# Performance work log

Measured on AMD Instinct MI355X. Metric: run time of the kernel, lower is better.

Reference implementation:

```python
import jax, jax.numpy as jnp
import numpy as np

B, N, DIN, DOUT = 8, 2048, 512, 256
NUM_BUCKETS = 20


def setup_inputs() -> dict:
    key = jax.random.key(0)
    ks = jax.random.split(key, 12)
    s_in = 1.0 / np.sqrt(DIN)
    s_out = 1.0 / np.sqrt(DOUT)
    return {
        "x": jax.random.normal(ks[0], (B, N, DIN), dtype=jnp.float32),
        "price_rank": jax.random.randint(ks[1], (B, N), 0, N, dtype=jnp.int64),
        "Wq": jax.random.uniform(ks[2], (DOUT, DIN), jnp.float32, -s_in, s_in),
        "bq": jax.random.uniform(ks[3], (DOUT,), jnp.float32, -s_in, s_in),
        "Wk": jax.random.uniform(ks[4], (DOUT, DIN), jnp.float32, -s_in, s_in),
        "bk": jax.random.uniform(ks[5], (DOUT,), jnp.float32, -s_in, s_in),
        "Wv": jax.random.uniform(ks[6], (DOUT, DIN), jnp.float32, -s_in, s_in),
        "bv": jax.random.uniform(ks[7], (DOUT,), jnp.float32, -s_in, s_in),
        "Ws": jax.random.uniform(ks[8], (1, DOUT), jnp.float32, -s_out, s_out),
        "bs": jax.random.uniform(ks[9], (1,), jnp.float32, -s_out, s_out),
        "rank_emb": jax.random.normal(ks[10], (NUM_BUCKETS, 1), dtype=jnp.float32),
        "rank_w": jnp.ones((1,), dtype=jnp.float32),
    }


def reference(x, price_rank, Wq, bq, Wk, bk, Wv, bv, Ws, bs, rank_emb, rank_w):
    scale = jnp.sqrt(jnp.asarray(DOUT, dtype=x.dtype))
    q = jnp.einsum("bnd,od->bno", x, Wq) + bq  # [B,N,DOUT]
    k = jnp.einsum("bnd,od->bno", x, Wk) + bk
    v = jnp.einsum("bnd,od->bno", x, Wv) + bv
    scores = jnp.einsum("bno,bmo->bnm", q, k) / scale  # [B,N,N]
    # learned pairwise rank-distance bias gate
    rank_dist = jnp.abs(price_rank[:, :, None] - price_rank[:, None, :])
    buckets = jnp.clip(rank_dist // 5, 0, NUM_BUCKETS - 1)  # [B,N,N] int
    prior = rank_emb[buckets, 0]  # gather embedding, squeeze last dim
    gate = jax.nn.sigmoid(rank_w[0] * prior)
    scores = scores * gate
    attn = jax.nn.softmax(scores, axis=2)
    context = jnp.einsum("bnm,bmo->bno", attn, v)  # [B,N,DOUT]
    winner = jax.nn.sigmoid(jnp.einsum("bno,uo->bnu", context, Ws) + bs)[..., 0]
    return winner  # [B,N]
```

## Files before the change

### kernel.cpp

```cpp
#include <hip/hip_runtime.h>
#include <hip/hip_bf16.h>

#define B_    8
#define N_    2048
#define DIN_  512
#define DOUT_ 256
#define NBUCK 20

typedef __attribute__((ext_vector_type(8))) short  short8;
typedef __attribute__((ext_vector_type(4))) float  floatx4;

__device__ __forceinline__ unsigned short f2b(float f) {
    __hip_bfloat16 h = __float2bfloat16(f);
    unsigned short u;
    __builtin_memcpy(&u, &h, 2);
    return u;
}

__device__ __forceinline__ void load_lds16(const unsigned short* g, unsigned short* l) {
    __builtin_amdgcn_global_load_lds(
        (const __attribute__((address_space(1))) unsigned int*)g,
        (__attribute__((address_space(3))) unsigned int*)l, 16, 0, 0);
}

__device__ __forceinline__ float fexp2(float x) {
    float r;
    asm("v_exp_f32 %0, %1" : "=v"(r) : "v"(x));
    return r;
}

__global__ __launch_bounds__(256) void prep_kernel(
    const float* __restrict__ Wv, const float* __restrict__ Ws,
    const float* __restrict__ bv,
    float* __restrict__ wvs, float* __restrict__ bvs) {
    const int blk = blockIdx.x, tid = threadIdx.x;
    __shared__ float wsl[DOUT_];
    wsl[tid] = Ws[tid];
    __syncthreads();
    if (tid < 128) {
        int d = blk * 128 + tid;
        float s0 = 0.f, s1 = 0.f, s2 = 0.f, s3 = 0.f;
#pragma unroll 8
        for (int o = 0; o < DOUT_; o += 4) {
            s0 += Wv[(size_t)(o + 0) * DIN_ + d] * wsl[o + 0];
            s1 += Wv[(size_t)(o + 1) * DIN_ + d] * wsl[o + 1];
            s2 += Wv[(size_t)(o + 2) * DIN_ + d] * wsl[o + 2];
            s3 += Wv[(size_t)(o + 3) * DIN_ + d] * wsl[o + 3];
        }
        wvs[d] = (s0 + s1) + (s2 + s3);
    }
    if (blk == 0 && tid < 64) {
        float bb = wsl[tid] * bv[tid] + wsl[tid + 64] * bv[tid + 64] +
                   wsl[tid + 128] * bv[tid + 128] + wsl[tid + 192] * bv[tid + 192];
        for (int off = 1; off < 64; off <<= 1) bb += __shfl_xor(bb, off, 64);
        if (tid == 0) *bvs = bb;
    }
}

__global__ __launch_bounds__(256) void cvt_x_kernel(const float* __restrict__ x,
                                                    const float* __restrict__ wvs,
                                                    const float* __restrict__ bvs,
                                                    const float* __restrict__ wq,
                                                    const float* __restrict__ wk,
                                                    unsigned short* __restrict__ xb,
                                                    unsigned short* __restrict__ wdst,
                                                    float* __restrict__ vw) {
    int tid = threadIdx.x;
    if (blockIdx.x >= 4096) {
        int i = ((blockIdx.x - 4096) * 256 + tid) * 8;
        const float* src = (i < 131072) ? (wq + i) : (wk + (i - 131072));
        float4 a = *(const float4*)(src);
        float4 b = *(const float4*)(src + 4);
        uint4 r;
        r.x = f2b(a.x) | ((unsigned)f2b(a.y) << 16);
        r.y = f2b(a.z) | ((unsigned)f2b(a.w) << 16);
        r.z = f2b(b.x) | ((unsigned)f2b(b.y) << 16);
        r.w = f2b(b.z) | ((unsigned)f2b(b.w) << 16);
        *(uint4*)(wdst + i) = r;
        return;
    }
    int wave = tid >> 6, lane = tid & 63;
    int row = blockIdx.x * 4 + wave;
    size_t base = (size_t)row * DIN_ + lane * 8;
    float4 a = *(const float4*)(x + base);
    float4 b = *(const float4*)(x + base + 4);
    float4 wa = *(const float4*)(wvs + lane * 8);
    float4 wb = *(const float4*)(wvs + lane * 8 + 4);
    uint4 r;
    r.x = f2b(a.x) | ((unsigned)f2b(a.y) << 16);
    r.y = f2b(a.z) | ((unsigned)f2b(a.w) << 16);
    r.z = f2b(b.x) | ((unsigned)f2b(b.y) << 16);
    r.w = f2b(b.z) | ((unsigned)f2b(b.w) << 16);
    *(uint4*)(xb + base) = r;
    float d = a.x * wa.x + a.y * wa.y + a.z * wa.z + a.w * wa.w +
              b.x * wb.x + b.y * wb.y + b.z * wb.z + b.w * wb.w;
    for (int off = 1; off < 64; off <<= 1) d += __shfl_xor(d, off, 64);
    if (lane == 0) vw[row] = d + *bvs;
}

__global__ __launch_bounds__(256, 2) void qkv_kernel(
    const unsigned short* __restrict__ xb, const unsigned short* __restrict__ wb,
    const float* __restrict__ bq, const float* __restrict__ bk,
    unsigned short* __restrict__ qo, unsigned short* __restrict__ ko) {
    __shared__ unsigned short alds[2][128 * 64];
    __shared__ unsigned short blds[2][128 * 64];
    const int g = blockIdx.x;
    const int xcd = g & 7, t2 = g >> 3;
    const int colBlk = t2 & 3, rowGrp = t2 >> 2;
    const int rowBlk = rowGrp * 8 + xcd;
    const int tid = threadIdx.x;
    const int wave = tid >> 6, lane = tid & 63, quad = lane >> 4, l16 = lane & 15;
    const int wr = wave >> 1, wc = wave & 1;
    const int row0 = rowBlk * 128, col0 = colBlk * 128;
    const int sw3 = l16 & 7;

    floatx4 acc[4][4];
#pragma unroll
    for (int i = 0; i < 4; ++i)
#pragma unroll
        for (int j = 0; j < 4; ++j) acc[i][j] = (floatx4){0.f, 0.f, 0.f, 0.f};

    const int gseg = (lane & 7) ^ (lane >> 3);
    const unsigned short* ag = xb + (size_t)(row0 + wave * 8 + (lane >> 3)) * DIN_ + gseg * 8;
    const unsigned short* bg = wb + (size_t)(col0 + wave * 8 + (lane >> 3)) * DIN_ + gseg * 8;

#pragma unroll
    for (int i = 0; i < 4; ++i) {
        load_lds16(ag + (size_t)i * 32 * DIN_, &alds[0][wave * 512 + i * 2048]);
        load_lds16(bg + (size_t)i * 32 * DIN_, &blds[0][wave * 512 + i * 2048]);
    }
    __syncthreads();

#pragma unroll 1
    for (int t = 0; t < 8; ++t) {
        const unsigned short* al = (t & 1) ? alds[1] : alds[0];
        const unsigned short* bl = (t & 1) ? blds[1] : blds[0];
        unsigned short* aln = (t & 1) ? &alds[0][0] : &alds[1][0];
        unsigned short* bln = (t & 1) ? &blds[0][0] : &blds[1][0];
        if (t < 7) {
            size_t koff = (size_t)(t + 1) * 64;
#pragma unroll
            for (int i = 0; i < 4; ++i) {
                load_lds16(ag + (size_t)i * 32 * DIN_ + koff, aln + wave * 512 + i * 2048);
                load_lds16(bg + (size_t)i * 32 * DIN_ + koff, bln + wave * 512 + i * 2048);
            }
        }
#pragma unroll
        for (int h = 0; h < 2; ++h) {
            short8 af[4], bf[4];
#pragma unroll
            for (int f = 0; f < 4; ++f) {
                int ar = wr * 64 + f * 16 + l16;
                int br = wc * 64 + f * 16 + l16;
                int s  = (h * 4 + quad) ^ sw3;
                af[f] = *(const short8*)&al[(size_t)ar * 64 + s * 8];
                bf[f] = *(const short8*)&bl[(size_t)br * 64 + s * 8];
            }
#pragma unroll
            for (int i = 0; i < 4; ++i)
#pragma unroll
                for (int j = 0; j < 4; ++j)
                    acc[i][j] = __builtin_amdgcn_mfma_f32_16x16x32_bf16(af[i], bf[j], acc[i][j], 0, 0, 0);
        }
        __syncthreads();
    }

#pragma unroll
    for (int j = 0; j < 4; ++j) {
        int col = col0 + wc * 64 + j * 16 + l16;
        unsigned short* dst = (col < 256) ? qo : ko;
        float bias = (col < 256) ? bq[col] : bk[col - 256];
        int c = col & 255;
#pragma unroll
        for (int i = 0; i < 4; ++i)
#pragma unroll
            for (int r = 0; r < 4; ++r) {
                int row = row0 + wr * 64 + i * 16 + quad * 4 + r;
                dst[(size_t)row * DOUT_ + c] = f2b(acc[i][j][r] + bias);
            }
    }
}

__global__ __launch_bounds__(512, 2) void attn_kernel(
    const unsigned short* __restrict__ q, const unsigned short* __restrict__ k,
    const float* __restrict__ vw, const int* __restrict__ pr,
    const float* __restrict__ rank_emb, const float* __restrict__ rank_w,
    const float* __restrict__ bs, float* __restrict__ out) {
    const int g = blockIdx.x;
    const int b = g & 7, rblk = g >> 3;
    const int tid = threadIdx.x, wave = tid >> 6, lane = tid & 63;
    const int quad = lane >> 4, l16 = lane & 15;
    const int n0 = rblk * 64;
    const int sw = l16 & 7;

    __shared__ unsigned short klds[2][8][4096];
    __shared__ float gtab[NBUCK];
    __shared__ float lL[8][64], wdL[8][64];

    if (tid < NBUCK)
        gtab[tid] = 0.0625f * 1.44269504f / (1.f + __expf(-rank_w[0] * rank_emb[tid]));
    __syncthreads();

    const unsigned short* qb = q + (size_t)b * N_ * DOUT_;
    const unsigned short* kb = k + (size_t)b * N_ * DOUT_;
    const float* vwb = vw + b * N_;
    const int* prb = pr + b * N_;

    short8 qf[4][8];
#pragma unroll
    for (int a = 0; a < 4; ++a)
#pragma unroll
        for (int c = 0; c < 8; ++c)
            qf[a][c] = *(const short8*)(qb + (size_t)(n0 + a * 16 + l16) * DOUT_ + c * 32 + quad * 8);

    float prn5[4][4];
#pragma unroll
    for (int a = 0; a < 4; ++a)
#pragma unroll
        for (int r = 0; r < 4; ++r)
            prn5[a][r] = (float)prb[n0 + a * 16 + quad * 4 + r] * 0.2f;

    float lacc[4][4], wacc[4][4];
#pragma unroll
    for (int a = 0; a < 4; ++a)
#pragma unroll
        for (int r = 0; r < 4; ++r) { lacc[a][r] = 0.f; wacc[a][r] = 0.f; }

    const int srow = lane >> 5;
    const int spos = lane & 31;
    const unsigned short* kwb = kb + (size_t)(wave * 16) * DOUT_;
    unsigned short* buf0 = &klds[0][wave][0];
    unsigned short* buf1 = &klds[1][wave][0];
    const int colbase = wave * 16 + l16;

    int   prm_raw = prb[colbase];
    float vwv_cur = vwb[colbase];

#pragma unroll
    for (int i = 0; i < 8; ++i) {
        int row = i * 2 + srow;
        int gseg = spos ^ (row & 7);
        load_lds16(kwb + (size_t)row * DOUT_ + gseg * 8, buf0 + i * 512);
    }

#pragma unroll 1
    for (int j = 0; j < 16; ++j) {
        unsigned short* bufc = (j & 1) ? buf1 : buf0;
        unsigned short* bufn = (j & 1) ? buf0 : buf1;

        floatx4 s[4];
#pragma unroll
        for (int a = 0; a < 4; ++a) s[a] = (floatx4){0.f, 0.f, 0.f, 0.f};
        __builtin_amdgcn_s_setprio(1);
#pragma unroll
        for (int c = 0; c < 8; ++c) {
            int seg = (quad + 4 * c) ^ sw;
            short8 kf = *(const short8*)&bufc[((size_t)l16 * 32 + seg) * 8];
            s[0] = __builtin_amdgcn_mfma_f32_16x16x32_bf16(qf[0][c], kf, s[0], 0, 0, 0);
            s[1] = __builtin_amdgcn_mfma_f32_16x16x32_bf16(qf[1][c], kf, s[1], 0, 0, 0);
            s[2] = __builtin_amdgcn_mfma_f32_16x16x32_bf16(qf[2][c], kf, s[2], 0, 0, 0);
            s[3] = __builtin_amdgcn_mfma_f32_16x16x32_bf16(qf[3][c], kf, s[3], 0, 0, 0);
        }
        __builtin_amdgcn_s_setprio(0);
        int nxtcol = ((j < 15) ? (j + 1) * 128 : j * 128) + colbase;
        int   prm_nxt = prb[nxtcol];
        float vwv_nxt = vwb[nxtcol];
        if (j < 15) {
            const unsigned short* src = kwb + (size_t)(j + 1) * 128 * DOUT_;
#pragma unroll
            for (int i = 0; i < 8; ++i) {
                int row = i * 2 + srow;
                int gseg = spos ^ (row & 7);
                load_lds16(src + (size_t)row * DOUT_ + gseg * 8, bufn + i * 512);
            }
        }
        float prm5 = (float)prm_raw * 0.2f;
#pragma unroll
        for (int a = 0; a < 4; ++a)
#pragma unroll
            for (int r = 0; r < 4; ++r) {
                float d5 = fabsf(prn5[a][r] - prm5);
                int idx = (int)fminf(d5, 19.0f);
                float p = fexp2(s[a][r] * gtab[idx]);
                lacc[a][r] += p;
                wacc[a][r] += p * vwv_cur;
            }
        prm_raw = prm_nxt;
        vwv_cur = vwv_nxt;
    }

#pragma unroll
    for (int off = 1; off < 16; off <<= 1) {
#pragma unroll
        for (int a = 0; a < 4; ++a)
#pragma unroll
            for (int r = 0; r < 4; ++r) {
                lacc[a][r] += __shfl_xor(lacc[a][r], off, 64);
                wacc[a][r] += __shfl_xor(wacc[a][r], off, 64);
            }
    }
    if (l16 == 0) {
#pragma unroll
        for (int a = 0; a < 4; ++a)
#pragma unroll
            for (int r = 0; r < 4; ++r) {
                int row = a * 16 + quad * 4 + r;
                lL[wave][row]  = lacc[a][r];
                wdL[wave][row] = wacc[a][r];
            }
    }
    __syncthreads();
    if (tid < 64) {
        float l = 0.f, wd = 0.f;
#pragma unroll
        for (int s2 = 0; s2 < 8; ++s2) { l += lL[s2][tid]; wd += wdL[s2][tid]; }
        float logit = wd / l + bs[0];
        out[(size_t)b * N_ + n0 + tid] = 1.f / (1.f + __expf(-logit));
    }
}

extern "C" void kernel_launch(void* const* d_in, const int* in_sizes, int n_in,
                              void* d_out, int out_size, void* d_ws, size_t ws_size,
                              hipStream_t stream) {
    const float* x   = (const float*)d_in[0];
    const int*   pr  = (const int*)d_in[1];
    const float* Wq  = (const float*)d_in[2];
    const float* bq  = (const float*)d_in[3];
    const float* Wk  = (const float*)d_in[4];
    const float* bk  = (const float*)d_in[5];
    const float* Wv  = (const float*)d_in[6];
    const float* bv  = (const float*)d_in[7];
    const float* Ws  = (const float*)d_in[8];
    const float* bs  = (const float*)d_in[9];
    const float* remb = (const float*)d_in[10];
    const float* rw   = (const float*)d_in[11];
    float* out = (float*)d_out;

    char* ws = (char*)d_ws;
    unsigned short* xb  = (unsigned short*)ws;
    unsigned short* wb  = (unsigned short*)(ws + 16777216);
    unsigned short* q   = (unsigned short*)(ws + 17301504);
    unsigned short* kk  = (unsigned short*)(ws + 25690112);
    float*          vwp = (float*)(ws + 34078720);
    float*          wvs = (float*)(ws + 34144256);
    float*          bvs = (float*)(ws + 34146304);

    hipLaunchKernelGGL(prep_kernel, dim3(4), dim3(256), 0, stream,
                       Wv, Ws, bv, wvs, bvs);
    hipLaunchKernelGGL(cvt_x_kernel, dim3(4224), dim3(256), 0, stream,
                       x, wvs, bvs, Wq, Wk, xb, wb, vwp);
    hipLaunchKernelGGL(qkv_kernel, dim3(512), dim3(256), 0, stream,
                       xb, wb, bq, bk, q, kk);
    hipLaunchKernelGGL(attn_kernel, dim3(256), dim3(512), 0, stream,
                       q, kk, vwp, pr, remb, rw, bs, out);
    hipLaunchKernelGGL(attn_kernel, dim3(256), dim3(512), 0, stream,
                       q, kk, vwp, pr, remb, rw, bs, out);
}
```

Before: 178.2 us.

## Software-pipeline QK MFMA with gate/exp and drop duplicate attention launch

```diff
diff --git a/kernel.cpp b/kernel.cpp
--- a/kernel.cpp
+++ b/kernel.cpp
@@ -233,22 +233,16 @@
     unsigned short* buf1 = &klds[1][wave][0];
     const int colbase = wave * 16 + l16;
 
-    int   prm_raw = prb[colbase];
-    float vwv_cur = vwb[colbase];
-
-#pragma unroll
-    for (int i = 0; i < 8; ++i) {
-        int row = i * 2 + srow;
-        int gseg = spos ^ (row & 7);
-        load_lds16(kwb + (size_t)row * DOUT_ + gseg * 8, buf0 + i * 512);
-    }
-
-#pragma unroll 1
-    for (int j = 0; j < 16; ++j) {
-        unsigned short* bufc = (j & 1) ? buf1 : buf0;
-        unsigned short* bufn = (j & 1) ? buf0 : buf1;
-
-        floatx4 s[4];
+    auto stage = [&](int j, unsigned short* buf) {
+        const unsigned short* src = kwb + (size_t)j * 128 * DOUT_;
+#pragma unroll
+        for (int i = 0; i < 8; ++i) {
+            int row = i * 2 + srow;
+            int gseg = spos ^ (row & 7);
+            load_lds16(src + (size_t)row * DOUT_ + gseg * 8, buf + i * 512);
+        }
+    };
+    auto mfma = [&](floatx4 (&s)[4], const unsigned short* bufc) {
 #pragma unroll
         for (int a = 0; a < 4; ++a) s[a] = (floatx4){0.f, 0.f, 0.f, 0.f};
         __builtin_amdgcn_s_setprio(1);
@@ -262,18 +256,8 @@
             s[3] = __builtin_amdgcn_mfma_f32_16x16x32_bf16(qf[3][c], kf, s[3], 0, 0, 0);
         }
         __builtin_amdgcn_s_setprio(0);
-        int nxtcol = ((j < 15) ? (j + 1) * 128 : j * 128) + colbase;
-        int   prm_nxt = prb[nxtcol];
-        float vwv_nxt = vwb[nxtcol];
-        if (j < 15) {
-            const unsigned short* src = kwb + (size_t)(j + 1) * 128 * DOUT_;
-#pragma unroll
-            for (int i = 0; i < 8; ++i) {
-                int row = i * 2 + srow;
-                int gseg = spos ^ (row & 7);
-                load_lds16(src + (size_t)row * DOUT_ + gseg * 8, bufn + i * 512);
-            }
-        }
+    };
+    auto gate = [&](floatx4 (&s)[4], int prm_raw, float vwv) {
         float prm5 = (float)prm_raw * 0.2f;
 #pragma unroll
         for (int a = 0; a < 4; ++a)
@@ -283,11 +267,47 @@
                 int idx = (int)fminf(d5, 19.0f);
                 float p = fexp2(s[a][r] * gtab[idx]);
                 lacc[a][r] += p;
-                wacc[a][r] += p * vwv_cur;
-            }
-        prm_raw = prm_nxt;
-        vwv_cur = vwv_nxt;
-    }
+                wacc[a][r] += p * vwv;
+            }
+    };
+
+    floatx4 sA[4], sB[4];
+
+    int   prm_a = prb[colbase];
+    float vw_a  = vwb[colbase];
+    stage(0, buf0);
+    int   prm_b = prb[128 + colbase];
+    float vw_b  = vwb[128 + colbase];
+    stage(1, buf1);
+    mfma(sA, buf0);
+
+#pragma unroll 1
+    for (int jj = 0; jj < 7; ++jj) {
+        {
+            int jn = 2 * jj + 2;
+            int   prm_c = prb[jn * 128 + colbase];
+            float vw_c  = vwb[jn * 128 + colbase];
+            stage(jn, buf0);
+            mfma(sB, buf1);
+            __builtin_amdgcn_sched_barrier(0);
+            gate(sA, prm_a, vw_a);
+            prm_a = prm_c; vw_a = vw_c;
+        }
+        {
+            int jn = 2 * jj + 3;
+            int   prm_c = prb[jn * 128 + colbase];
+            float vw_c  = vwb[jn * 128 + colbase];
+            stage(jn, buf1);
+            mfma(sA, buf0);
+            __builtin_amdgcn_sched_barrier(0);
+            gate(sB, prm_b, vw_b);
+            prm_b = prm_c; vw_b = vw_c;
+        }
+    }
+    mfma(sB, buf1);
+    __builtin_amdgcn_sched_barrier(0);
+    gate(sA, prm_a, vw_a);
+    gate(sB, prm_b, vw_b);
 
 #pragma unroll
     for (int off = 1; off < 16; off <<= 1) {
@@ -353,6 +373,4 @@
                        xb, wb, bq, bk, q, kk);
     hipLaunchKernelGGL(attn_kernel, dim3(256), dim3(512), 0, stream,
                        q, kk, vwp, pr, remb, rw, bs, out);
-    hipLaunchKernelGGL(attn_kernel, dim3(256), dim3(512), 0, stream,
-                       q, kk, vwp, pr, remb, rw, bs, out);
-}
+}
```

Result: slower. 216.7 us (+21.6%).
